# Kernel tuning notes

Measured on AMD Instinct MI355X. Metric: run time of the kernel, lower is better.

The kernel has to match this reference:

```python
import jax, jax.numpy as jnp
import numpy as np

VERY_NEG = -1e30

H = 768           # hidden_size
A_DIM = 768       # attention_dim_size
N_TREE = 40000    # num_tree_nodes (embed_init vocab)
N_CODES = 10000   # number of leaf codes (rows of leaves_list)
MAX_ANC = 8       # max ancestors per code
B, V, M = 16, 32, 48  # batch, visits, codes per visit
OUT = 512         # classifier output_size


def setup_inputs() -> dict:
    key = jax.random.key(0)
    ks = jax.random.split(key, 12)
    leaves_list = jax.random.randint(ks[0], (N_CODES, MAX_ANC), 0, N_TREE)
    ancestors_list = jax.random.randint(ks[1], (N_CODES, MAX_ANC), 0, N_TREE)
    masks = (jax.random.uniform(ks[2], (N_CODES, MAX_ANC)) > 0.3).astype(jnp.float32)
    masks = masks.at[:, 0].set(1.0)  # ensure at least one valid ancestor
    input_ids = jax.random.randint(ks[3], (B, V, M), 0, N_CODES + 1)  # 0 is padding row
    code_mask = (jax.random.uniform(ks[4], (B, V, M)) > 0.2).astype(jnp.float32)
    code_mask = code_mask.at[:, :, 0].set(1.0)
    s = 1.0 / np.sqrt(H)
    embed_table = jax.random.normal(ks[5], (N_TREE, H), dtype=jnp.float32) * s
    w1 = jax.random.normal(ks[6], (2 * H, A_DIM), dtype=jnp.float32) * (1.0 / np.sqrt(2 * H))
    b1 = jnp.zeros((A_DIM,), dtype=jnp.float32)
    w2 = jax.random.normal(ks[7], (A_DIM, 1), dtype=jnp.float32) * (1.0 / np.sqrt(A_DIM))
    b2 = jnp.zeros((1,), dtype=jnp.float32)
    wc = jax.random.normal(ks[8], (H, OUT), dtype=jnp.float32) * s
    bc = jnp.zeros((OUT,), dtype=jnp.float32)
    return {
        "embed_table": embed_table, "w1": w1, "b1": b1, "w2": w2, "b2": b2,
        "wc": wc, "bc": bc, "masks": masks, "code_mask": code_mask,
        "leaves_list": leaves_list, "ancestors_list": ancestors_list,
        "input_ids": input_ids,
    }


def reference(embed_table, w1, b1, w2, b2, wc, bc, masks, code_mask,
              leaves_list, ancestors_list, input_ids):
    # --- DAGAttention2D over ancestor axis ---
    leaves = embed_table[leaves_list]        # [N, A, H]
    ancestors = embed_table[ancestors_list]  # [N, A, H]
    m = masks[:, :, None]                    # [N, A, 1]
    x = jnp.concatenate([leaves * m, ancestors * m], axis=-1)  # [N, A, 2H]
    x = jax.nn.relu(jnp.einsum('nah,hd->nad', x, w1) + b1)
    x = jnp.einsum('nad,do->nao', x, w2) + b2                  # [N, A, 1]
    x = x + (1.0 - m) * VERY_NEG
    attn = jax.nn.softmax(x, axis=1)                           # softmax over ancestors
    dag_emb = (attn * ancestors * m).sum(axis=1)               # [N, H]
    # --- dict_matrix with padding row 0, embedding lookup ---
    dict_matrix = jnp.concatenate([jnp.zeros((1, dag_emb.shape[1]), dag_emb.dtype), dag_emb], axis=0)
    emb = dict_matrix[input_ids]             # [B, V, M, H]
    cm = code_mask[..., None]
    pooled = (emb * cm).sum(axis=2) / jnp.clip(cm.sum(axis=2), 1.0, None)  # [B, V, H]
    # --- Classifier (dropout inactive at eval, activation=None) ---
    out = jnp.einsum('bvh,ho->bvo', pooled, wc) + bc           # [B, V, OUT]
    return out
```

## Files before the change

### kernel.cpp

```cpp
#include <hip/hip_runtime.h>
#include <stdint.h>

typedef unsigned short u16;
typedef __bf16 bfx8 __attribute__((ext_vector_type(8)));
typedef float f32x4 __attribute__((ext_vector_type(4)));
typedef u16 u16x8 __attribute__((ext_vector_type(8)));

#define HD 768
#define NTREE 40000
#define NCODES 10000
#define GNN 1536
#define OUTD 512
#define NBV 512
#define VNEG (-1e30f)
#define TB 4

#define BM 256
#define BN 256
#define BK 64
#define NKT (HD / BK)
#define NMT ((NTREE + BM - 1) / BM)
#define NNT (GNN / BN)
#define GRID (NMT * NNT)
#define Q8 (GRID / 8)
#define R8 (GRID % 8)

#define WAITV(n) asm volatile("s_waitcnt vmcnt(" #n ")" ::: "memory")

__device__ __forceinline__ float bf2f(u16 u) {
  union { uint32_t i; float f; } v; v.i = ((uint32_t)u) << 16; return v.f;
}
__device__ __forceinline__ u16 f2bf(float f) {
  union { float fl; uint32_t i; } v; v.fl = f;
  uint32_t u = v.i;
  u += 0x7FFFu + ((u >> 16) & 1u);
  return (u16)(u >> 16);
}

__global__ void k_convE(const float* __restrict__ E, u16* __restrict__ Ebf, int n4) {
  int i = blockIdx.x * blockDim.x + threadIdx.x;
  if (i >= n4) return;
  float4 v = ((const float4*)E)[i];
  ushort4 r;
  r.x = f2bf(v.x); r.y = f2bf(v.y); r.z = f2bf(v.z); r.w = f2bf(v.w);
  ((ushort4*)Ebf)[i] = r;
}

__global__ void k_bt(const float* __restrict__ w1, u16* __restrict__ Bt) {
  int idx = blockIdx.x * blockDim.x + threadIdx.x;
  if (idx >= GNN * HD) return;
  int n = idx / HD, k = idx % HD;
  int srow = k + ((n >= HD) ? HD : 0);
  int scol = (n >= HD) ? (n - HD) : n;
  Bt[idx] = f2bf(w1[(size_t)srow * HD + scol]);
}

__global__ __launch_bounds__(512, 2) void k_gemm(const u16* __restrict__ A,
                                                 const u16* __restrict__ B,
                                                 u16* __restrict__ C) {
  __shared__ u16 lds[65536];

  const int tid    = threadIdx.x;
  const int lane   = tid & 63;
  const int wv     = tid >> 6;
  const int wm     = wv >> 2;
  const int wn2    = wv & 3;
  const int lane15 = lane & 15;
  const int g      = lane >> 4;

  const int orig = blockIdx.x;
  const int xcd = orig & 7, lin = orig >> 3;
  const int wg = (xcd < R8 ? xcd * (Q8 + 1) : R8 * (Q8 + 1) + (xcd - R8) * Q8) + lin;
  const int mt = wg / NNT, nt = wg % NNT;
  const int tm = mt * BM, tn = nt * BN;

  const u16* aSrc[2][2];
  const u16* bSrc[2][2];
#pragma unroll
  for (int u = 0; u < 2; ++u) {
    const int o    = u * 8192 + tid * 16;
    const int rloc = o >> 7;
    const int c    = ((o >> 4) & 7) ^ (rloc & 7);
#pragma unroll
    for (int h = 0; h < 2; ++h) {
      int ra = tm + h * 128 + rloc; if (ra > NTREE - 1) ra = NTREE - 1;
      aSrc[u][h] = A + (size_t)ra * HD + c * 8;
      bSrc[u][h] = B + (size_t)(tn + h * 128 + rloc) * HD + c * 8;
    }
  }

#define STAGE_A(MH, NB, TT) do {                                               \
    _Pragma("unroll") for (int u = 0; u < 2; ++u)                              \
      __builtin_amdgcn_global_load_lds(                                        \
        (const __attribute__((address_space(1))) void*)(aSrc[u][MH] + (TT) * BK), \
        (__attribute__((address_space(3))) void*)((char*)lds + (NB) * 32768 +  \
            (MH) * 16384 + u * 8192 + tid * 16),                               \
        16, 0, 0);                                                             \
  } while (0)

#define STAGE_B(NH, NB, TT) do {                                               \
    _Pragma("unroll") for (int u = 0; u < 2; ++u)                              \
      __builtin_amdgcn_global_load_lds(                                        \
        (const __attribute__((address_space(1))) void*)(bSrc[u][NH] + (TT) * BK), \
        (__attribute__((address_space(3))) void*)((char*)lds + 65536 +         \
            (NB) * 32768 + (NH) * 16384 + u * 8192 + tid * 16),                \
        16, 0, 0);                                                             \
  } while (0)

  f32x4 acc[8][4];
#pragma unroll
  for (int i = 0; i < 8; ++i)
#pragma unroll
    for (int j = 0; j < 4; ++j) acc[i][j] = (f32x4){0.f, 0.f, 0.f, 0.f};

  int colz[2];
  colz[0] = ((0 * 4 + g) ^ (lane15 & 7)) * 8;
  colz[1] = ((1 * 4 + g) ^ (lane15 & 7)) * 8;
  const int aBase = (wm * 128 + lane15) * 64;
  const int bBase = (wn2 * 64 + lane15) * 64;

  bfx8 aF[4], bF[4];

#define PHASE(MH, KS, STAGE_STMT, DRAIN_STMT)                                  \
  {                                                                            \
    const int _az = bA + aBase + (MH) * 4096 + colz[KS];                       \
    _Pragma("unroll") for (int i = 0; i < 4; ++i)                              \
      aF[i] = *(const bfx8*)&lds[_az + i * 1024];                              \
    if ((MH) == 0) {                                                           \
      const int _bz = bB + bBase + colz[KS];                                   \
      _Pragma("unroll") for (int j = 0; j < 4; ++j)                            \
        bF[j] = *(const bfx8*)&lds[_bz + j * 1024];                            \
    }                                                                          \
    STAGE_STMT;                                                                \
    __builtin_amdgcn_s_barrier();                                              \
    asm volatile("s_waitcnt lgkmcnt(0)" ::: "memory");                         \
    __builtin_amdgcn_sched_barrier(0);                                         \
    __builtin_amdgcn_s_setprio(1);                                             \
    _Pragma("unroll") for (int i = 0; i < 4; ++i)                              \
      _Pragma("unroll") for (int j = 0; j < 4; ++j)                            \
        acc[(MH) * 4 + i][j] = __builtin_amdgcn_mfma_f32_16x16x32_bf16(        \
            aF[i], bF[j], acc[(MH) * 4 + i][j], 0, 0, 0);                      \
    __builtin_amdgcn_s_setprio(0);                                             \
    DRAIN_STMT;                                                                \
    __builtin_amdgcn_s_barrier();                                              \
  }

  STAGE_A(0, 0, 0);
  STAGE_A(1, 0, 0);
  STAGE_B(0, 0, 0);
  STAGE_B(1, 0, 0);
  WAITV(0);
  __builtin_amdgcn_s_barrier();

  for (int t = 0; t < NKT; ++t) {
    const int cur = t & 1, nb = cur ^ 1;
    const int bA = cur * 16384;
    const int bB = 32768 + cur * 16384;
    const bool more = (t + 1 < NKT);

    PHASE(0, 0, if (more) { STAGE_A(0, nb, t + 1); STAGE_A(1, nb, t + 1); }, );
    PHASE(1, 0, if (more) { STAGE_B(0, nb, t + 1); STAGE_B(1, nb, t + 1); }, );
    PHASE(0, 1, , );
    PHASE(1, 1, , WAITV(0));
  }

  const int r0 = (lane >> 4) * 4, cc = lane15;
#pragma unroll
  for (int mf = 0; mf < 8; ++mf) {
#pragma unroll
    for (int nf = 0; nf < 4; ++nf) {
#pragma unroll
      for (int rr = 0; rr < 4; ++rr) {
        const int row = tm + wm * 128 + mf * 16 + r0 + rr;
        if (row < NTREE) {
          const int col = tn + wn2 * 64 + nf * 16 + cc;
          C[(size_t)row * GNN + col] = f2bf(acc[mf][nf][rr]);
        }
      }
    }
  }
#undef PHASE
#undef STAGE_A
#undef STAGE_B
}

__device__ __forceinline__ float dot8(const u16* pr, const u16* qr,
                                      const float* b1, const float* w2, int d) {
  u16x8 pv = *(const u16x8*)(pr + d);
  u16x8 qv = *(const u16x8*)(qr + d);
  float4 bb0 = *(const float4*)(b1 + d);
  float4 bb1 = *(const float4*)(b1 + d + 4);
  float4 ww0 = *(const float4*)(w2 + d);
  float4 ww1 = *(const float4*)(w2 + d + 4);
  float s = 0.f, v;
  v = fmaxf(bf2f(pv[0]) + bf2f(qv[0]) + bb0.x, 0.f); s += v * ww0.x;
  v = fmaxf(bf2f(pv[1]) + bf2f(qv[1]) + bb0.y, 0.f); s += v * ww0.y;
  v = fmaxf(bf2f(pv[2]) + bf2f(qv[2]) + bb0.z, 0.f); s += v * ww0.z;
  v = fmaxf(bf2f(pv[3]) + bf2f(qv[3]) + bb0.w, 0.f); s += v * ww0.w;
  v = fmaxf(bf2f(pv[4]) + bf2f(qv[4]) + bb1.x, 0.f); s += v * ww1.x;
  v = fmaxf(bf2f(pv[5]) + bf2f(qv[5]) + bb1.y, 0.f); s += v * ww1.y;
  v = fmaxf(bf2f(pv[6]) + bf2f(qv[6]) + bb1.z, 0.f); s += v * ww1.z;
  v = fmaxf(bf2f(pv[7]) + bf2f(qv[7]) + bb1.w, 0.f); s += v * ww1.w;
  return s;
}

__global__ __launch_bounds__(512) void k_attn(const u16* __restrict__ PQ,
                                              const u16* __restrict__ Ebf,
                                              const float* __restrict__ b1,
                                              const float* __restrict__ w2,
                                              const float* __restrict__ b2,
                                              const float* __restrict__ masks,
                                              const int* __restrict__ leaves,
                                              const int* __restrict__ anc,
                                              float* __restrict__ dag) {
  const int n = blockIdx.x;
  const int tid = threadIdx.x, lane = tid & 63, wv = tid >> 6;
  __shared__ float sc[8];
  __shared__ float m_s[8];
  __shared__ int   an_s[8];
  __shared__ int   lv_s[8];
  if (tid < 8) {
    an_s[tid] = anc[n * 8 + tid];
    lv_s[tid] = leaves[n * 8 + tid];
    m_s[tid]  = masks[n * 8 + tid];
  }
  __syncthreads();

  {
    const int a = wv;
    const float mm = m_s[a];
    if (mm == 0.f) {
      if (lane == 0) sc[a] = VNEG;
    } else {
      const int l = lv_s[a], an = an_s[a];
      const u16* pr = PQ + (size_t)l * GNN;
      const u16* qr = PQ + (size_t)an * GNN + HD;
      float s = dot8(pr, qr, b1, w2, lane * 8);
      if (lane < 32) s += dot8(pr, qr, b1, w2, 512 + lane * 8);
#pragma unroll
      for (int off = 32; off > 0; off >>= 1) s += __shfl_down(s, off);
      if (lane == 0) sc[a] = s + b2[0];
    }
  }
  __syncthreads();

  float mx = sc[0];
#pragma unroll
  for (int a = 1; a < 8; ++a) mx = fmaxf(mx, sc[a]);
  float ex[8], den = 0.f;
#pragma unroll
  for (int a = 0; a < 8; ++a) { ex[a] = expf(sc[a] - mx); den += ex[a]; }
  const float inv = 1.0f / den;
  float cf[8];
#pragma unroll
  for (int a = 0; a < 8; ++a) cf[a] = ex[a] * inv * m_s[a];

  {
    int d = tid;
    float accv = 0.f;
#pragma unroll
    for (int a = 0; a < 8; ++a) {
      const float cfa = cf[a];
      if (cfa != 0.f) accv += cfa * bf2f(Ebf[(size_t)an_s[a] * HD + d]);
    }
    dag[(size_t)n * HD + d] = accv;
  }
  if (tid < 256) {
    const int d = 512 + tid;
    float accv = 0.f;
#pragma unroll
    for (int a = 0; a < 8; ++a) {
      const float cfa = cf[a];
      if (cfa != 0.f) accv += cfa * bf2f(Ebf[(size_t)an_s[a] * HD + d]);
    }
    dag[(size_t)n * HD + d] = accv;
  }
}

__global__ __launch_bounds__(256) void k_pool(const float* __restrict__ dag,
                                              const int* __restrict__ ids,
                                              const float* __restrict__ cm,
                                              float* __restrict__ pooled) {
  const int bv = blockIdx.x, tid = threadIdx.x;
  __shared__ int   id_s[48];
  __shared__ float cm_s[48];
  if (tid < 48) { id_s[tid] = ids[bv * 48 + tid]; cm_s[tid] = cm[bv * 48 + tid]; }
  __syncthreads();
  float cnt = 0.f;
  for (int m = 0; m < 48; ++m) cnt += cm_s[m];
  const float scale = 1.0f / fmaxf(cnt, 1.0f);
  if (tid < 192) {
    float4 accv = make_float4(0.f, 0.f, 0.f, 0.f);
    for (int m = 0; m < 48; ++m) {
      const int id = id_s[m];
      const float cv = cm_s[m];
      if (id > 0 && cv != 0.f) {
        float4 v = *(const float4*)(dag + (size_t)(id - 1) * HD + tid * 4);
        accv.x += cv * v.x; accv.y += cv * v.y;
        accv.z += cv * v.z; accv.w += cv * v.w;
      }
    }
    accv.x *= scale; accv.y *= scale; accv.z *= scale; accv.w *= scale;
    *(float4*)(pooled + (size_t)bv * HD + tid * 4) = accv;
  }
}

__global__ __launch_bounds__(256) void k_out(const float* __restrict__ pooled,
                                             const float* __restrict__ wc,
                                             const float* __restrict__ bc,
                                             float* __restrict__ out) {
  const int b0 = blockIdx.x * TB;
  const int tid = threadIdx.x;
  __shared__ float pl[TB][HD];
  for (int i = tid; i < TB * HD; i += 256) pl[i / HD][i % HD] = pooled[(size_t)b0 * HD + i];
  __syncthreads();
  float a0[TB], a1[TB];
#pragma unroll
  for (int r = 0; r < TB; ++r) { a0[r] = 0.f; a1[r] = 0.f; }
  for (int h = 0; h < HD; ++h) {
    const float w0  = wc[(size_t)h * OUTD + tid];
    const float w1v = wc[(size_t)h * OUTD + tid + 256];
#pragma unroll
    for (int r = 0; r < TB; ++r) { const float p = pl[r][h]; a0[r] += p * w0; a1[r] += p * w1v; }
  }
  const float bc0 = bc[tid], bc1 = bc[tid + 256];
#pragma unroll
  for (int r = 0; r < TB; ++r) {
    out[(size_t)(b0 + r) * OUTD + tid]       = a0[r] + bc0;
    out[(size_t)(b0 + r) * OUTD + tid + 256] = a1[r] + bc1;
  }
}

extern "C" void kernel_launch(void* const* d_in, const int* in_sizes, int n_in,
                              void* d_out, int out_size, void* d_ws, size_t ws_size,
                              hipStream_t stream) {
  const float* E     = (const float*)d_in[0];
  const float* w1    = (const float*)d_in[1];
  const float* b1    = (const float*)d_in[2];
  const float* w2    = (const float*)d_in[3];
  const float* b2    = (const float*)d_in[4];
  const float* wc    = (const float*)d_in[5];
  const float* bc    = (const float*)d_in[6];
  const float* masks = (const float*)d_in[7];
  const float* cm    = (const float*)d_in[8];
  const int*   leaves = (const int*)d_in[9];
  const int*   anc    = (const int*)d_in[10];
  const int*   ids    = (const int*)d_in[11];
  float* out = (float*)d_out;

  if (n_in < 12) return;
  if (in_sizes[0] != NTREE * HD) return;
  if (out_size != NBV * OUTD) return;

  char* ws = (char*)d_ws;
  const size_t szEbf = (size_t)NTREE * HD * 2;
  const size_t szBt  = (size_t)GNN * HD * 2;
  const size_t szPQ  = (size_t)NTREE * GNN * 2;
  const size_t szDag = (size_t)NCODES * HD * 4;
  const size_t szPl  = (size_t)NBV * HD * 4;
  if (ws_size < szEbf + szBt + szPQ + szDag + szPl) return;

  u16*   Ebf    = (u16*)ws;            ws += szEbf;
  u16*   Bt     = (u16*)ws;            ws += szBt;
  u16*   PQ     = (u16*)ws;            ws += szPQ;
  float* dag    = (float*)ws;          ws += szDag;
  float* pooled = (float*)ws;          ws += szPl;

  const int n4 = NTREE * HD / 4;
  k_convE<<<(n4 + 255) / 256, 256, 0, stream>>>(E, Ebf, n4);
  k_bt<<<(GNN * HD + 255) / 256, 256, 0, stream>>>(w1, Bt);
  k_gemm<<<GRID, 512, 0, stream>>>(Ebf, Bt, PQ);
  k_attn<<<NCODES, 512, 0, stream>>>(PQ, Ebf, b1, w2, b2, masks, leaves, anc, dag);
  k_pool<<<NBV, 256, 0, stream>>>(dag, ids, cm, pooled);
  k_out<<<NBV / TB, 256, 0, stream>>>(pooled, wc, bc, out);
}
```

Baseline: 301.7 us.

## Software-pipeline LDS fragment reads across MFMA phases in GEMM main loop

Restructures the GEMM K-loop so the A/B fragments for the next phase are read from LDS into a second register set while the current MFMA batch runs. Partial lgkmcnt waits replace the full drains, and one barrier per phase is removed. Global source pointers become 32-bit offsets to save registers. The attention score dot product is also reworked so all 64 lanes each handle 12 elements, instead of lanes doing uneven 8+8 work. The cost is more VGPRs for the doubled fragment buffers and more delicate synchronization that depends on the exact waitcnt counts.

```diff
diff --git a/kernel.cpp b/kernel.cpp
--- a/kernel.cpp
+++ b/kernel.cpp
@@ -4,7 +4,6 @@
 typedef unsigned short u16;
 typedef __bf16 bfx8 __attribute__((ext_vector_type(8)));
 typedef float f32x4 __attribute__((ext_vector_type(4)));
-typedef u16 u16x8 __attribute__((ext_vector_type(8)));
 
 #define HD 768
 #define NTREE 40000
@@ -26,6 +25,7 @@
 #define R8 (GRID % 8)
 
 #define WAITV(n) asm volatile("s_waitcnt vmcnt(" #n ")" ::: "memory")
+#define LGKM(n)  asm volatile("s_waitcnt lgkmcnt(" #n ")" ::: "memory")
 
 __device__ __forceinline__ float bf2f(u16 u) {
   union { uint32_t i; float f; } v; v.i = ((uint32_t)u) << 16; return v.f;
@@ -74,8 +74,7 @@
   const int mt = wg / NNT, nt = wg % NNT;
   const int tm = mt * BM, tn = nt * BN;
 
-  const u16* aSrc[2][2];
-  const u16* bSrc[2][2];
+  uint32_t aOff[2][2], bOff[2][2];
 #pragma unroll
   for (int u = 0; u < 2; ++u) {
     const int o    = u * 8192 + tid * 16;
@@ -84,15 +83,15 @@
 #pragma unroll
     for (int h = 0; h < 2; ++h) {
       int ra = tm + h * 128 + rloc; if (ra > NTREE - 1) ra = NTREE - 1;
-      aSrc[u][h] = A + (size_t)ra * HD + c * 8;
-      bSrc[u][h] = B + (size_t)(tn + h * 128 + rloc) * HD + c * 8;
+      aOff[u][h] = (uint32_t)ra * HD + c * 8;
+      bOff[u][h] = (uint32_t)(tn + h * 128 + rloc) * HD + c * 8;
     }
   }
 
 #define STAGE_A(MH, NB, TT) do {                                               \
     _Pragma("unroll") for (int u = 0; u < 2; ++u)                              \
       __builtin_amdgcn_global_load_lds(                                        \
-        (const __attribute__((address_space(1))) void*)(aSrc[u][MH] + (TT) * BK), \
+        (const __attribute__((address_space(1))) void*)(A + aOff[u][MH] + (TT) * BK), \
         (__attribute__((address_space(3))) void*)((char*)lds + (NB) * 32768 +  \
             (MH) * 16384 + u * 8192 + tid * 16),                               \
         16, 0, 0);                                                             \
@@ -101,7 +100,7 @@
 #define STAGE_B(NH, NB, TT) do {                                               \
     _Pragma("unroll") for (int u = 0; u < 2; ++u)                              \
       __builtin_amdgcn_global_load_lds(                                        \
-        (const __attribute__((address_space(1))) void*)(bSrc[u][NH] + (TT) * BK), \
+        (const __attribute__((address_space(1))) void*)(B + bOff[u][NH] + (TT) * BK), \
         (__attribute__((address_space(3))) void*)((char*)lds + 65536 +         \
             (NB) * 32768 + (NH) * 16384 + u * 8192 + tid * 16),                \
         16, 0, 0);                                                             \
@@ -119,31 +118,28 @@
   const int aBase = (wm * 128 + lane15) * 64;
   const int bBase = (wn2 * 64 + lane15) * 64;
 
-  bfx8 aF[4], bF[4];
-
-#define PHASE(MH, KS, STAGE_STMT, DRAIN_STMT)                                  \
-  {                                                                            \
-    const int _az = bA + aBase + (MH) * 4096 + colz[KS];                       \
+  bfx8 aF0[4], aF1[4], bF0[4], bF1[4];
+
+#define READ_A(DST, MH, KS, BA) do {                                           \
+    const int _a = (BA) + aBase + (MH) * 4096 + colz[KS];                      \
     _Pragma("unroll") for (int i = 0; i < 4; ++i)                              \
-      aF[i] = *(const bfx8*)&lds[_az + i * 1024];                              \
-    if ((MH) == 0) {                                                           \
-      const int _bz = bB + bBase + colz[KS];                                   \
-      _Pragma("unroll") for (int j = 0; j < 4; ++j)                            \
-        bF[j] = *(const bfx8*)&lds[_bz + j * 1024];                            \
-    }                                                                          \
-    STAGE_STMT;                                                                \
-    __builtin_amdgcn_s_barrier();                                              \
-    asm volatile("s_waitcnt lgkmcnt(0)" ::: "memory");                         \
-    __builtin_amdgcn_sched_barrier(0);                                         \
+      DST[i] = *(const bfx8*)&lds[_a + i * 1024];                              \
+  } while (0)
+
+#define READ_B(DST, KS, BB) do {                                               \
+    const int _b = (BB) + bBase + colz[KS];                                    \
+    _Pragma("unroll") for (int j = 0; j < 4; ++j)                              \
+      DST[j] = *(const bfx8*)&lds[_b + j * 1024];                              \
+  } while (0)
+
+#define MFMA16(MH, AFR, BFR) do {                                              \
     __builtin_amdgcn_s_setprio(1);                                             \
     _Pragma("unroll") for (int i = 0; i < 4; ++i)                              \
       _Pragma("unroll") for (int j = 0; j < 4; ++j)                            \
         acc[(MH) * 4 + i][j] = __builtin_amdgcn_mfma_f32_16x16x32_bf16(        \
-            aF[i], bF[j], acc[(MH) * 4 + i][j], 0, 0, 0);                      \
+            AFR[i], BFR[j], acc[(MH) * 4 + i][j], 0, 0, 0);                    \
     __builtin_amdgcn_s_setprio(0);                                             \
-    DRAIN_STMT;                                                                \
-    __builtin_amdgcn_s_barrier();                                              \
-  }
+  } while (0)
 
   STAGE_A(0, 0, 0);
   STAGE_A(1, 0, 0);
@@ -151,17 +147,49 @@
   STAGE_B(1, 0, 0);
   WAITV(0);
   __builtin_amdgcn_s_barrier();
+  READ_A(aF0, 0, 0, 0);
+  READ_B(bF0, 0, 32768);
 
   for (int t = 0; t < NKT; ++t) {
-    const int cur = t & 1, nb = cur ^ 1;
-    const int bA = cur * 16384;
-    const int bB = 32768 + cur * 16384;
+    const int bA  = (t & 1) * 16384;
+    const int bB  = 32768 + (t & 1) * 16384;
+    const int nb  = (t + 1) & 1;
+    const int nbA = nb * 16384;
+    const int nbB = 32768 + nb * 16384;
     const bool more = (t + 1 < NKT);
 
-    PHASE(0, 0, if (more) { STAGE_A(0, nb, t + 1); STAGE_A(1, nb, t + 1); }, );
-    PHASE(1, 0, if (more) { STAGE_B(0, nb, t + 1); STAGE_B(1, nb, t + 1); }, );
-    PHASE(0, 1, , );
-    PHASE(1, 1, , WAITV(0));
+    READ_A(aF1, 1, 0, bA);
+    if (more) { STAGE_A(0, nb, t + 1); STAGE_A(1, nb, t + 1); }
+    LGKM(4);
+    __builtin_amdgcn_sched_barrier(0);
+    MFMA16(0, aF0, bF0);
+    __builtin_amdgcn_s_barrier();
+
+    READ_A(aF0, 0, 1, bA);
+    READ_B(bF1, 1, bB);
+    if (more) { STAGE_B(0, nb, t + 1); STAGE_B(1, nb, t + 1); }
+    LGKM(8);
+    __builtin_amdgcn_sched_barrier(0);
+    MFMA16(1, aF1, bF0);
+    __builtin_amdgcn_s_barrier();
+
+    READ_A(aF1, 1, 1, bA);
+    LGKM(4);
+    __builtin_amdgcn_sched_barrier(0);
+    MFMA16(0, aF0, bF1);
+    WAITV(0);
+    __builtin_amdgcn_s_barrier();
+
+    if (more) {
+      READ_A(aF0, 0, 0, nbA);
+      READ_B(bF0, 0, nbB);
+      LGKM(8);
+    } else {
+      LGKM(0);
+    }
+    __builtin_amdgcn_sched_barrier(0);
+    MFMA16(1, aF1, bF1);
+    __builtin_amdgcn_s_barrier();
   }
 
   const int r0 = (lane >> 4) * 4, cc = lane15;
@@ -179,29 +207,11 @@
       }
     }
   }
-#undef PHASE
+#undef MFMA16
+#undef READ_A
+#undef READ_B
 #undef STAGE_A
 #undef STAGE_B
-}
-
-__device__ __forceinline__ float dot8(const u16* pr, const u16* qr,
-                                      const float* b1, const float* w2, int d) {
-  u16x8 pv = *(const u16x8*)(pr + d);
-  u16x8 qv = *(const u16x8*)(qr + d);
-  float4 bb0 = *(const float4*)(b1 + d);
-  float4 bb1 = *(const float4*)(b1 + d + 4);
-  float4 ww0 = *(const float4*)(w2 + d);
-  float4 ww1 = *(const float4*)(w2 + d + 4);
-  float s = 0.f, v;
-  v = fmaxf(bf2f(pv[0]) + bf2f(qv[0]) + bb0.x, 0.f); s += v * ww0.x;
-  v = fmaxf(bf2f(pv[1]) + bf2f(qv[1]) + bb0.y, 0.f); s += v * ww0.y;
-  v = fmaxf(bf2f(pv[2]) + bf2f(qv[2]) + bb0.z, 0.f); s += v * ww0.z;
-  v = fmaxf(bf2f(pv[3]) + bf2f(qv[3]) + bb0.w, 0.f); s += v * ww0.w;
-  v = fmaxf(bf2f(pv[4]) + bf2f(qv[4]) + bb1.x, 0.f); s += v * ww1.x;
-  v = fmaxf(bf2f(pv[5]) + bf2f(qv[5]) + bb1.y, 0.f); s += v * ww1.y;
-  v = fmaxf(bf2f(pv[6]) + bf2f(qv[6]) + bb1.z, 0.f); s += v * ww1.z;
-  v = fmaxf(bf2f(pv[7]) + bf2f(qv[7]) + bb1.w, 0.f); s += v * ww1.w;
-  return s;
 }
 
 __global__ __launch_bounds__(512) void k_attn(const u16* __restrict__ PQ,
@@ -235,8 +245,21 @@
       const int l = lv_s[a], an = an_s[a];
       const u16* pr = PQ + (size_t)l * GNN;
       const u16* qr = PQ + (size_t)an * GNN + HD;
-      float s = dot8(pr, qr, b1, w2, lane * 8);
-      if (lane < 32) s += dot8(pr, qr, b1, w2, 512 + lane * 8);
+      const int d0 = lane * 12;
+      float s = 0.f;
+#pragma unroll
+      for (int jj = 0; jj < 3; ++jj) {
+        const int d = d0 + jj * 4;
+        ushort4 pv = *(const ushort4*)(pr + d);
+        ushort4 qv = *(const ushort4*)(qr + d);
+        float4  bb = *(const float4*)(b1 + d);
+        float4  ww = *(const float4*)(w2 + d);
+        float v;
+        v = fmaxf(bf2f(pv.x) + bf2f(qv.x) + bb.x, 0.f); s += v * ww.x;
+        v = fmaxf(bf2f(pv.y) + bf2f(qv.y) + bb.y, 0.f); s += v * ww.y;
+        v = fmaxf(bf2f(pv.z) + bf2f(qv.z) + bb.z, 0.f); s += v * ww.z;
+        v = fmaxf(bf2f(pv.w) + bf2f(qv.w) + bb.w, 0.f); s += v * ww.w;
+      }
 #pragma unroll
       for (int off = 32; off > 0; off >>= 1) s += __shfl_down(s, off);
       if (lane == 0) sc[a] = s + b2[0];
@@ -256,7 +279,7 @@
   for (int a = 0; a < 8; ++a) cf[a] = ex[a] * inv * m_s[a];
 
   {
-    int d = tid;
+    const int d = tid;
     float accv = 0.f;
 #pragma unroll
     for (int a = 0; a < 8; ++a) {
```

After: 303.0 us. Within noise of the previous version (+0.5%).
